# Kernel tuning notes

Measured on AMD Instinct MI355X. Metric: run time of the kernel, lower is better.

The kernel has to match this reference:

```python
import jax, jax.numpy as jnp
import numpy as np

D_MODEL = 1024
N_HEADS = 16
HEAD_DIM = 64
D_FF = 4096


def rmsnorm(x, w):
    eps = jnp.finfo(x.dtype).eps
    var = jnp.mean(jnp.square(x), axis=-1, keepdims=True)
    return x * jax.lax.rsqrt(var + eps) * w


def setup_inputs() -> dict:
    key = jax.random.key(0)
    ks = jax.random.split(key, 8)
    d, h, hd, dff = D_MODEL, N_HEADS, HEAD_DIM, D_FF
    s = 0.02
    return {
        "x": jax.random.normal(ks[0], (2, 2048, d), dtype=jnp.float32),
        "norm_w": jnp.ones((d,), dtype=jnp.float32),
        "Wq": jax.random.normal(ks[1], (d, h * hd), dtype=jnp.float32) * s,
        "Wk": jax.random.normal(ks[2], (d, h * hd), dtype=jnp.float32) * s,
        "Wv": jax.random.normal(ks[3], (d, h * hd), dtype=jnp.float32) * s,
        "Wo": jax.random.normal(ks[4], (h * hd, d), dtype=jnp.float32) * s,
        "W1": jax.random.normal(ks[5], (d, dff), dtype=jnp.float32) * s,
        "W2": jax.random.normal(ks[6], (dff, d), dtype=jnp.float32) * s,
    }


def reference(x, norm_w, Wq, Wk, Wv, Wo, W1, W2):
    B, T, d = x.shape
    h, hd = N_HEADS, HEAD_DIM
    scale = 1.0 / np.sqrt(hd)

    xn = rmsnorm(x, norm_w)

    # attention branch
    q = (xn @ Wq).reshape(B, T, h, hd).transpose(0, 2, 1, 3)  # [B,h,T,hd]
    k = (xn @ Wk).reshape(B, T, h, hd).transpose(0, 2, 1, 3)
    v = (xn @ Wv).reshape(B, T, h, hd).transpose(0, 2, 1, 3)
    attn = jnp.einsum("bhqd,bhkd->bhqk", q, k) * scale
    causal = jnp.tril(jnp.ones((T, T), dtype=bool))
    attn = jnp.where(causal, attn, -jnp.inf)
    attn = jax.nn.softmax(attn, axis=-1)
    out = jnp.einsum("bhqk,bhkd->bhqd", attn, v)
    out = out.transpose(0, 2, 1, 3).reshape(B, T, h * hd)
    attn_out = out @ Wo

    # FFN branch
    ffn_out = jax.nn.silu(xn @ W1) @ W2

    return x + attn_out + ffn_out
```

## Files before the change

### kernel.cpp

```cpp
#include <hip/hip_runtime.h>

#define DM   1024
#define DFF  4096
#define NH   16
#define HD   64
#define TT   2048
#define BT   4096
#define KC   5120

typedef unsigned short u16;
typedef unsigned int   u32;
typedef __attribute__((ext_vector_type(8))) short s16x8;
typedef __attribute__((ext_vector_type(4))) float f32x4;

__device__ __forceinline__ u16 f2bf(float f) {
  u32 u = __builtin_bit_cast(u32, f);
  u += 0x7fffu + ((u >> 16) & 1u);
  return (u16)(u >> 16);
}

__device__ __forceinline__ void gl2lds16(const void* g, void* l) {
  __builtin_amdgcn_global_load_lds((__attribute__((address_space(1))) void*)(g),
                                   (__attribute__((address_space(3))) void*)(l),
                                   16, 0, 0);
}

__global__ __launch_bounds__(256) void rmsnorm_k(const float* __restrict__ x,
                                                 const float* __restrict__ w,
                                                 u16* __restrict__ xn) {
  const int row = blockIdx.x;
  const int t = threadIdx.x;
  const float4 v = ((const float4*)(x + (size_t)row * DM))[t];
  float ss = v.x*v.x + v.y*v.y + v.z*v.z + v.w*v.w;
  #pragma unroll
  for (int off = 32; off; off >>= 1) ss += __shfl_xor(ss, off, 64);
  __shared__ float red[4];
  if ((t & 63) == 0) red[t >> 6] = ss;
  __syncthreads();
  const float tot = red[0] + red[1] + red[2] + red[3];
  const float r = __builtin_amdgcn_rsqf(tot * (1.0f / DM) + 1.1920929e-7f);
  const float4 wv = ((const float4*)w)[t];
  u16* o = xn + (size_t)row * DM + t * 4;
  o[0] = f2bf(v.x * r * wv.x);
  o[1] = f2bf(v.y * r * wv.y);
  o[2] = f2bf(v.z * r * wv.z);
  o[3] = f2bf(v.w * r * wv.w);
}

__global__ __launch_bounds__(256) void wtrans_k(const float* __restrict__ W,
                                                u16* __restrict__ Wt,
                                                int K, int N, int pitch, int koff) {
  __shared__ float tile[32][33];
  const int n0 = blockIdx.x * 32, k0 = blockIdx.y * 32;
  const int tx = threadIdx.x, ty = threadIdx.y;
  #pragma unroll
  for (int i = 0; i < 4; ++i)
    tile[ty + i*8][tx] = W[(size_t)(k0 + ty + i*8) * N + n0 + tx];
  __syncthreads();
  #pragma unroll
  for (int i = 0; i < 4; ++i)
    Wt[(size_t)(n0 + ty + i*8) * pitch + koff + k0 + tx] = f2bf(tile[tx][ty + i*8]);
}

__global__ __launch_bounds__(256, 2) void gemm_fused(const u16* __restrict__ A,
                                                     const u16* __restrict__ Bt,
                                                     u16* __restrict__ qkb,
                                                     u16* __restrict__ vtg,
                                                     u16* __restrict__ acat) {
  const int K = 1024;
  __shared__ u16 sA[2 * 128 * 32];
  __shared__ u16 sB[2 * 128 * 32];
  const int t = threadIdx.x;
  const int lane = t & 63, wave = t >> 6;
  const int quad = lane >> 4, l4 = lane & 15;
  const int wy = wave >> 1, wx = wave & 1;
  const size_t mBase = (size_t)blockIdx.y * 128;
  const size_t nBase = (size_t)blockIdx.x * 128;
  const int r  = t >> 2;
  const int c8 = ((t & 3) ^ ((t >> 3) & 3)) * 8;
  const int qsw = (quad ^ ((l4 >> 1) & 3)) * 8;
  const u16* Ag0 = A + (mBase + r) * K + c8;
  const u16* Ag1 = Ag0 + (size_t)64 * K;
  const u16* Bg0 = Bt + (nBase + r) * K + c8;
  const u16* Bg1 = Bg0 + (size_t)64 * K;
  char* sAb = (char*)sA + (wave << 10);
  char* sBb = (char*)sB + (wave << 10);

  f32x4 acc[4][4];
  #pragma unroll
  for (int i = 0; i < 4; ++i)
    #pragma unroll
    for (int j = 0; j < 4; ++j)
      acc[i][j] = (f32x4)0.0f;

  auto issue = [&](int bf, int k0) {
    gl2lds16(Ag0 + k0, sAb + bf*8192);
    gl2lds16(Ag1 + k0, sAb + bf*8192 + 4096);
    gl2lds16(Bg0 + k0, sBb + bf*8192);
    gl2lds16(Bg1 + k0, sBb + bf*8192 + 4096);
  };

  issue(0, 0);
  for (int kt = 0; kt < 32; ++kt) {
    const int bf = kt & 1;
    __syncthreads();
    if (kt + 1 < 32) issue(bf ^ 1, (kt + 1) * 32);
    const u16* pA = sA + bf * 4096;
    const u16* pB = sB + bf * 4096;
    s16x8 af[4], bfr[4];
    #pragma unroll
    for (int i = 0; i < 4; ++i)
      af[i] = *(const s16x8*)&pA[(wy*64 + i*16 + l4) * 32 + qsw];
    #pragma unroll
    for (int j = 0; j < 4; ++j)
      bfr[j] = *(const s16x8*)&pB[(wx*64 + j*16 + l4) * 32 + qsw];
    #pragma unroll
    for (int i = 0; i < 4; ++i)
      #pragma unroll
      for (int j = 0; j < 4; ++j)
        acc[i][j] = __builtin_amdgcn_mfma_f32_16x16x32_bf16(af[i], bfr[j], acc[i][j], 0, 0, 0);
  }

  #pragma unroll
  for (int i = 0; i < 4; ++i) {
    const size_t row0 = mBase + wy*64 + i*16 + quad*4;
    #pragma unroll
    for (int j = 0; j < 4; ++j) {
      const int col = (int)nBase + wx*64 + j*16 + l4;
      if (nBase < 1024) {
        #pragma unroll
        for (int rg = 0; rg < 4; ++rg)
          qkb[(row0 + rg) * 2048 + col] = f2bf(acc[i][j][rg] * 0.18033688011f);
      } else if (nBase < 2048) {
        #pragma unroll
        for (int rg = 0; rg < 4; ++rg)
          qkb[(row0 + rg) * 2048 + col] = f2bf(acc[i][j][rg]);
      } else if (nBase < 3072) {
        const int cv = col - 2048, hh = cv >> 6, dd = cv & 63;
        const int bb = (int)(row0 >> 11), t0 = (int)(row0 & 2047);
        ushort4 pk;
        pk.x = f2bf(acc[i][j][0]); pk.y = f2bf(acc[i][j][1]);
        pk.z = f2bf(acc[i][j][2]); pk.w = f2bf(acc[i][j][3]);
        *(ushort4*)(vtg + ((size_t)((bb*16 + hh)*64 + dd)) * 2048 + t0) = pk;
      } else {
        #pragma unroll
        for (int rg = 0; rg < 4; ++rg) {
          float v = acc[i][j][rg];
          v = v / (1.0f + __expf(-v));
          acat[(row0 + rg) * (size_t)KC + 1024 + (col - 3072)] = f2bf(v);
        }
      }
    }
  }
}

__global__ __launch_bounds__(256, 2) void gemm_final(const u16* __restrict__ A,
                                                     const u16* __restrict__ Bt,
                                                     const float* __restrict__ x,
                                                     float* __restrict__ out) {
  __shared__ u16 sA[2 * 64 * 32];
  __shared__ u16 sB[2 * 128 * 32];
  const int t = threadIdx.x;
  const int lane = t & 63, wave = t >> 6;
  const int quad = lane >> 4, l4 = lane & 15;
  const int wy = wave >> 1, wx = wave & 1;
  const size_t mBase = (size_t)blockIdx.y * 64;
  const size_t nBase = (size_t)blockIdx.x * 128;
  const int r  = t >> 2;
  const int c8 = ((t & 3) ^ ((t >> 3) & 3)) * 8;
  const int qsw = (quad ^ ((l4 >> 1) & 3)) * 8;
  const u16* Ag  = A  + (mBase + r) * KC + c8;
  const u16* Bg0 = Bt + (nBase + r) * KC + c8;
  const u16* Bg1 = Bg0 + (size_t)64 * KC;
  char* sAb = (char*)sA + (wave << 10);
  char* sBb = (char*)sB + (wave << 10);

  f32x4 acc[2][4];
  #pragma unroll
  for (int i = 0; i < 2; ++i)
    #pragma unroll
    for (int j = 0; j < 4; ++j)
      acc[i][j] = (f32x4)0.0f;

  auto issue = [&](int bf, int k0) {
    gl2lds16(Ag  + k0, sAb + bf*4096);
    gl2lds16(Bg0 + k0, sBb + bf*8192);
    gl2lds16(Bg1 + k0, sBb + bf*8192 + 4096);
  };

  issue(0, 0);
  const int NIT = KC / 32;
  for (int kt = 0; kt < NIT; ++kt) {
    const int bf = kt & 1;
    __syncthreads();
    if (kt + 1 < NIT) issue(bf ^ 1, (kt + 1) * 32);
    const u16* pA = sA + bf * 2048;
    const u16* pB = sB + bf * 4096;
    s16x8 af[2], bfr[4];
    #pragma unroll
    for (int i = 0; i < 2; ++i)
      af[i] = *(const s16x8*)&pA[(wy*32 + i*16 + l4) * 32 + qsw];
    #pragma unroll
    for (int j = 0; j < 4; ++j)
      bfr[j] = *(const s16x8*)&pB[(wx*64 + j*16 + l4) * 32 + qsw];
    #pragma unroll
    for (int i = 0; i < 2; ++i)
      #pragma unroll
      for (int j = 0; j < 4; ++j)
        acc[i][j] = __builtin_amdgcn_mfma_f32_16x16x32_bf16(af[i], bfr[j], acc[i][j], 0, 0, 0);
  }

  #pragma unroll
  for (int i = 0; i < 2; ++i) {
    const size_t row0 = mBase + wy*32 + i*16 + quad*4;
    #pragma unroll
    for (int j = 0; j < 4; ++j) {
      const int col = (int)nBase + wx*64 + j*16 + l4;
      #pragma unroll
      for (int rg = 0; rg < 4; ++rg) {
        const size_t idx = (row0 + rg) * (size_t)DM + col;
        out[idx] = x[idx] + acc[i][j][rg];
      }
    }
  }
}

__global__ __launch_bounds__(128) void attn_k(const u16* __restrict__ qk,
                                              const u16* __restrict__ vtg,
                                              u16* __restrict__ acat) {
  const int bh = blockIdx.x, b = bh >> 4, h = bh & 15;
  const int qt = 63 - blockIdx.y;
  const int qw = qt * 32;
  const int wave = threadIdx.x >> 6, lane = threadIdx.x & 63;
  const int quad = lane >> 4, l4 = lane & 15;
  const u16* Qp = qk + (size_t)b * TT * 2048 + h * HD;
  const u16* Kp = Qp + 1024;
  const u16* Vp = vtg + (size_t)bh * 64 * 2048;

  __shared__ u16 Pb[2][32][72];
  __shared__ float Ob[32][68];
  __shared__ float Lb[32];

  s16x8 qf[2][2];
  #pragma unroll
  for (int mi = 0; mi < 2; ++mi)
    #pragma unroll
    for (int kf = 0; kf < 2; ++kf)
      qf[mi][kf] = *(const s16x8*)(Qp + (size_t)(qw + mi*16 + l4) * 2048 + kf*32 + quad*8);

  const s16x8 ones = {0x3F80,0x3F80,0x3F80,0x3F80,0x3F80,0x3F80,0x3F80,0x3F80};

  f32x4 o[2][4];
  f32x4 lacc[2];
  #pragma unroll
  for (int mi = 0; mi < 2; ++mi) {
    lacc[mi] = (f32x4)0.0f;
    #pragma unroll
    for (int ni = 0; ni < 4; ++ni) o[mi][ni] = (f32x4)0.0f;
  }

  const int n   = (qt + 2) >> 1;
  const int n0  = (n + 1) >> 1;
  const int kt0 = wave ? n0 : 0;
  const int kt1 = wave ? n : n0;

  for (int kt = kt0; kt < kt1; ++kt) {
    const int k0 = kt * 64;

    f32x4 st[4][2];
    #pragma unroll
    for (int nj = 0; nj < 4; ++nj) {
      const u16* kr = Kp + (size_t)(k0 + nj*16 + l4) * 2048 + quad*8;
      const s16x8 kf0 = *(const s16x8*)kr;
      const s16x8 kf1 = *(const s16x8*)(kr + 32);
      #pragma unroll
      for (int mi = 0; mi < 2; ++mi) {
        f32x4 a = (f32x4)0.0f;
        a = __builtin_amdgcn_mfma_f32_16x16x32_bf16(kf0, qf[mi][0], a, 0, 0, 0);
        a = __builtin_amdgcn_mfma_f32_16x16x32_bf16(kf1, qf[mi][1], a, 0, 0, 0);
        st[nj][mi] = a;
      }
    }

    s16x8 vb[2][4];
    #pragma unroll
    for (int kf2 = 0; kf2 < 2; ++kf2)
      #pragma unroll
      for (int ni = 0; ni < 4; ++ni)
        vb[kf2][ni] = *(const s16x8*)(Vp + (size_t)(ni*16 + l4) * 2048 + k0 + kf2*32 + quad*8);

    if (k0 + 63 > qw) {
      #pragma unroll
      for (int nj = 0; nj < 4; ++nj)
        #pragma unroll
        for (int mi = 0; mi < 2; ++mi)
          #pragma unroll
          for (int rg = 0; rg < 4; ++rg) {
            const int key = k0 + nj*16 + quad*4 + rg;
            const int q   = qw + mi*16 + l4;
            if (key > q) st[nj][mi][rg] = -1e30f;
          }
    }

    #pragma unroll
    for (int nj = 0; nj < 4; ++nj)
      #pragma unroll
      for (int mi = 0; mi < 2; ++mi) {
        float p0 = __builtin_amdgcn_exp2f(st[nj][mi][0]);
        float p1 = __builtin_amdgcn_exp2f(st[nj][mi][1]);
        float p2 = __builtin_amdgcn_exp2f(st[nj][mi][2]);
        float p3 = __builtin_amdgcn_exp2f(st[nj][mi][3]);
        uint2 w;
        w.x = __builtin_amdgcn_perm(__builtin_bit_cast(u32, p1),
                                    __builtin_bit_cast(u32, p0), 0x07060302u);
        w.y = __builtin_amdgcn_perm(__builtin_bit_cast(u32, p3),
                                    __builtin_bit_cast(u32, p2), 0x07060302u);
        *(uint2*)&Pb[wave][mi*16 + l4][nj*16 + quad*4] = w;
      }

    #pragma unroll
    for (int kf2 = 0; kf2 < 2; ++kf2) {
      s16x8 pa[2];
      #pragma unroll
      for (int mi = 0; mi < 2; ++mi)
        pa[mi] = *(const s16x8*)&Pb[wave][mi*16 + l4][kf2*32 + quad*8];
      #pragma unroll
      for (int mi = 0; mi < 2; ++mi) {
        lacc[mi] = __builtin_amdgcn_mfma_f32_16x16x32_bf16(pa[mi], ones, lacc[mi], 0, 0, 0);
        #pragma unroll
        for (int ni = 0; ni < 4; ++ni)
          o[mi][ni] = __builtin_amdgcn_mfma_f32_16x16x32_bf16(pa[mi], vb[kf2][ni], o[mi][ni], 0, 0, 0);
      }
    }
  }

  if (wave == 1) {
    #pragma unroll
    for (int mi = 0; mi < 2; ++mi)
      #pragma unroll
      for (int rg = 0; rg < 4; ++rg) {
        const int row = mi*16 + quad*4 + rg;
        #pragma unroll
        for (int ni = 0; ni < 4; ++ni) Ob[row][ni*16 + l4] = o[mi][ni][rg];
        if (l4 == 0) Lb[row] = lacc[mi][rg];
      }
  }
  __syncthreads();
  if (wave == 0) {
    #pragma unroll
    for (int mi = 0; mi < 2; ++mi)
      #pragma unroll
      for (int rg = 0; rg < 4; ++rg) {
        const int row = mi*16 + quad*4 + rg;
        const float inv = 1.0f / (lacc[mi][rg] + Lb[row]);
        #pragma unroll
        for (int ni = 0; ni < 4; ++ni)
          Pb[0][row][ni*16 + l4] = f2bf((o[mi][ni][rg] + Ob[row][ni*16 + l4]) * inv);
      }
    #pragma unroll
    for (int it = 0; it < 4; ++it) {
      const int row = it*8 + (lane >> 3);
      const int c0  = (lane & 7) * 8;
      const s16x8 pk = *(const s16x8*)&Pb[0][row][c0];
      *(s16x8*)(acat + ((size_t)b * TT + qw + row) * KC + h*HD + c0) = pk;
    }
  }
}

extern "C" void kernel_launch(void* const* d_in, const int* in_sizes, int n_in,
                              void* d_out, int out_size, void* d_ws, size_t ws_size,
                              hipStream_t stream) {
  (void)in_sizes; (void)n_in; (void)out_size; (void)ws_size;
  const float* x  = (const float*)d_in[0];
  const float* nw = (const float*)d_in[1];
  const float* Wq = (const float*)d_in[2];
  const float* Wk = (const float*)d_in[3];
  const float* Wv = (const float*)d_in[4];
  const float* Wo = (const float*)d_in[5];
  const float* W1 = (const float*)d_in[6];
  const float* W2 = (const float*)d_in[7];

  char* ws = (char*)d_ws;
  u16*   xn      = (u16*)(ws);
  u16*   wqkv1_t = (u16*)(ws + ((size_t)8  << 20));
  u16*   bcat    = (u16*)(ws + ((size_t)22 << 20));
  u16*   qkb     = (u16*)(ws + ((size_t)32 << 20));
  u16*   vtg     = (u16*)(ws + ((size_t)48 << 20));
  u16*   acat    = (u16*)(ws + ((size_t)56 << 20));
  float* dout    = (float*)d_out;

  rmsnorm_k<<<BT, 256, 0, stream>>>(x, nw, xn);
  const dim3 tb(32, 8);
  wtrans_k<<<dim3(32, 32),  tb, 0, stream>>>(Wq, wqkv1_t,                      1024, 1024, 1024, 0);
  wtrans_k<<<dim3(32, 32),  tb, 0, stream>>>(Wk, wqkv1_t + (size_t)1024*1024,  1024, 1024, 1024, 0);
  wtrans_k<<<dim3(32, 32),  tb, 0, stream>>>(Wv, wqkv1_t + (size_t)2048*1024,  1024, 1024, 1024, 0);
  wtrans_k<<<dim3(128, 32), tb, 0, stream>>>(W1, wqkv1_t + (size_t)3072*1024,  1024, 4096, 1024, 0);
  wtrans_k<<<dim3(32, 32),  tb, 0, stream>>>(Wo, bcat,                         1024, 1024, 5120, 0);
  wtrans_k<<<dim3(32, 128), tb, 0, stream>>>(W2, bcat,                         4096, 1024, 5120, 1024);

  gemm_fused<<<dim3(56, 32), 256, 0, stream>>>(xn, wqkv1_t, qkb, vtg, acat);
  attn_k<<<dim3(32, 64), 128, 0, stream>>>(qkb, vtg, acat);
  gemm_final<<<dim3(8, 64), 256, 0, stream>>>(acat, bcat, x, dout);
}
```

Before: 361.5 us.

## Deepen GEMM LDS pipeline to four stages with explicit vmcnt waits

Both GEMM kernels move from a double-buffered LDS scheme to a four-buffer ring that keeps three K-tiles of global-to-LDS loads in flight. Each iteration waits only until the oldest tile has landed, using an explicit s_waitcnt vmcnt count, then runs a raw barrier instead of __syncthreads, so memory latency is hidden behind more compute. The cost is doubled LDS use per block (64KB in gemm_fused), which may limit occupancy, and it relies on the hand-tuned vmcnt counts matching how many loads each issue emits.

```diff
diff --git a/kernel.cpp b/kernel.cpp
--- a/kernel.cpp
+++ b/kernel.cpp
@@ -24,6 +24,9 @@
                                    (__attribute__((address_space(3))) void*)(l),
                                    16, 0, 0);
 }
+
+#define S_BARRIER() do { __builtin_amdgcn_s_barrier(); __builtin_amdgcn_sched_barrier(0); } while (0)
+#define VMWAIT(n)   asm volatile("s_waitcnt vmcnt(" #n ")" ::: "memory")
 
 __global__ __launch_bounds__(256) void rmsnorm_k(const float* __restrict__ x,
                                                  const float* __restrict__ w,
@@ -68,8 +71,8 @@
                                                      u16* __restrict__ vtg,
                                                      u16* __restrict__ acat) {
   const int K = 1024;
-  __shared__ u16 sA[2 * 128 * 32];
-  __shared__ u16 sB[2 * 128 * 32];
+  __shared__ u16 sA[4 * 128 * 32];
+  __shared__ u16 sB[4 * 128 * 32];
   const int t = threadIdx.x;
   const int lane = t & 63, wave = t >> 6;
   const int quad = lane >> 4, l4 = lane & 15;
@@ -100,11 +103,7 @@
     gl2lds16(Bg1 + k0, sBb + bf*8192 + 4096);
   };
 
-  issue(0, 0);
-  for (int kt = 0; kt < 32; ++kt) {
-    const int bf = kt & 1;
-    __syncthreads();
-    if (kt + 1 < 32) issue(bf ^ 1, (kt + 1) * 32);
+  auto compute = [&](int bf) {
     const u16* pA = sA + bf * 4096;
     const u16* pB = sB + bf * 4096;
     s16x8 af[4], bfr[4];
@@ -119,7 +118,17 @@
       #pragma unroll
       for (int j = 0; j < 4; ++j)
         acc[i][j] = __builtin_amdgcn_mfma_f32_16x16x32_bf16(af[i], bfr[j], acc[i][j], 0, 0, 0);
-  }
+  };
+
+  issue(0, 0); issue(1, 32); issue(2, 64);
+  for (int kt = 0; kt < 30; ++kt) {
+    VMWAIT(8);
+    S_BARRIER();
+    if (kt + 3 < 32) issue((kt + 3) & 3, (kt + 3) * 32);
+    compute(kt & 3);
+  }
+  VMWAIT(4); S_BARRIER(); compute(30 & 3);
+  VMWAIT(0); S_BARRIER(); compute(31 & 3);
 
   #pragma unroll
   for (int i = 0; i < 4; ++i) {
@@ -158,8 +167,8 @@
                                                      const u16* __restrict__ Bt,
                                                      const float* __restrict__ x,
                                                      float* __restrict__ out) {
-  __shared__ u16 sA[2 * 64 * 32];
-  __shared__ u16 sB[2 * 128 * 32];
+  __shared__ u16 sA[4 * 64 * 32];
+  __shared__ u16 sB[4 * 128 * 32];
   const int t = threadIdx.x;
   const int lane = t & 63, wave = t >> 6;
   const int quad = lane >> 4, l4 = lane & 15;
@@ -188,12 +197,7 @@
     gl2lds16(Bg1 + k0, sBb + bf*8192 + 4096);
   };
 
-  issue(0, 0);
-  const int NIT = KC / 32;
-  for (int kt = 0; kt < NIT; ++kt) {
-    const int bf = kt & 1;
-    __syncthreads();
-    if (kt + 1 < NIT) issue(bf ^ 1, (kt + 1) * 32);
+  auto compute = [&](int bf) {
     const u16* pA = sA + bf * 2048;
     const u16* pB = sB + bf * 4096;
     s16x8 af[2], bfr[4];
@@ -208,7 +212,18 @@
       #pragma unroll
       for (int j = 0; j < 4; ++j)
         acc[i][j] = __builtin_amdgcn_mfma_f32_16x16x32_bf16(af[i], bfr[j], acc[i][j], 0, 0, 0);
-  }
+  };
+
+  const int NIT = KC / 32;
+  issue(0, 0); issue(1, 32); issue(2, 64);
+  for (int kt = 0; kt < NIT - 2; ++kt) {
+    VMWAIT(6);
+    S_BARRIER();
+    if (kt + 3 < NIT) issue((kt + 3) & 3, (kt + 3) * 32);
+    compute(kt & 3);
+  }
+  VMWAIT(3); S_BARRIER(); compute((NIT - 2) & 3);
+  VMWAIT(0); S_BARRIER(); compute((NIT - 1) & 3);
 
   #pragma unroll
   for (int i = 0; i < 2; ++i) {
```

After: 372.5 us. 3.0% more time.
